# Performance work log

Measured on AMD Instinct MI355X. Metric: run time of the kernel, lower is better.

The kernel has to match this reference:

```python
import jax, jax.numpy as jnp
import numpy as np

C = 1024      # channels
K = 7         # kernel_size
G = 1         # groups (G>1 crashes in the original torch code; see notes)
GC = C // G   # group_channels
OFFSET_SCALE = 2.0
LN_EPS = 1e-5


def setup_inputs() -> dict:
    key = jax.random.key(0)
    ks = jax.random.split(key, 8)
    N, L = 4, 2048
    s = 1.0 / np.sqrt(C)
    x = jax.random.normal(ks[0], (N, L, C), jnp.float32)
    Wi = jax.random.normal(ks[1], (C, C), jnp.float32) * s
    bi = jnp.zeros((C,), jnp.float32)
    dw_w = jax.random.normal(ks[2], (C, 1, 3), jnp.float32) * 0.5   # depthwise conv kernel (O, I/g=1, W)
    dw_b = jnp.zeros((C,), jnp.float32)
    ln_g = jnp.ones((C,), jnp.float32)
    ln_b = jnp.zeros((C,), jnp.float32)
    Wo = jax.random.normal(ks[3], (G * K, C), jnp.float32) * 0.02   # offset head (nonzero to exercise gather)
    bo = jnp.zeros((G * K,), jnp.float32)
    Wm = jax.random.normal(ks[4], (G * K, C), jnp.float32) * 0.02   # mask head
    bm = jnp.zeros((G * K,), jnp.float32)
    Wout = jax.random.normal(ks[5], (C, C), jnp.float32) * s
    bout = jnp.zeros((C,), jnp.float32)
    return {"x": x, "Wi": Wi, "bi": bi, "dw_w": dw_w, "dw_b": dw_b,
            "ln_g": ln_g, "ln_b": ln_b, "Wo": Wo, "bo": bo,
            "Wm": Wm, "bm": bm, "Wout": Wout, "bout": bout}


def _forward(x, Wi, bi, dw_w, dw_b, ln_g, ln_b, Wo, bo, Wm, bm, Wout, bout):
    N, L, Cc = x.shape
    dt = x.dtype
    # input projection
    x_proj = x @ Wi.T + bi                                  # [N,L,C]
    # depthwise conv (k=3, pad=1, groups=C) -> LayerNorm(C) -> GELU(exact)
    y = jax.lax.conv_general_dilated(
        x.transpose(0, 2, 1), dw_w, window_strides=(1,), padding=((1, 1),),
        dimension_numbers=("NCH", "OIH", "NCH"), feature_group_count=Cc)
    x_dw = y.transpose(0, 2, 1) + dw_b                       # [N,L,C]
    mu = x_dw.mean(-1, keepdims=True)
    var = ((x_dw - mu) ** 2).mean(-1, keepdims=True)
    x_dw = (x_dw - mu) * jax.lax.rsqrt(var + LN_EPS) * ln_g + ln_b
    x_dw = jax.nn.gelu(x_dw, approximate=False)
    # dynamic offsets and sampling mask
    offsets = (x_dw @ Wo.T + bo).reshape(N, L, G, K) * OFFSET_SCALE
    mask = jax.nn.softmax((x_dw @ Wm.T + bm).reshape(N, L, G, K), axis=-1)
    mask = jnp.nan_to_num(mask, nan=0.0)
    # absolute sampling positions
    ref_off = jnp.linspace(-(K // 2), K // 2, K).astype(dt)          # [K]
    pos = jnp.arange(L, dtype=dt)[None, :, None, None]               # [1,L,1,1]
    abs_pos = pos + ref_off[None, None, None, :] + offsets           # [N,L,G,K]
    apc = jnp.clip(abs_pos, 0.0, L - 1)
    p_floor = jnp.clip(apc.astype(jnp.int32), 0, L - 1)
    p_ceil = jnp.clip(p_floor + 1, 0, L - 1)
    w_ceil = apc - p_floor.astype(dt)
    w_floor = 1.0 - w_ceil
    valid = jnp.logical_not((abs_pos < 0) | (abs_pos > L - 1)).astype(dt)
    w_floor = w_floor * valid
    w_ceil = w_ceil * valid
    # gather + bilinear blend (G=1: each sample index grabs the full C channels)
    idx_f = p_floor.reshape(N, -1)[:, :, None]                       # [N, L*G*K, 1]
    idx_c = p_ceil.reshape(N, -1)[:, :, None]
    v_floor = jnp.take_along_axis(x_proj, idx_f, axis=1).reshape(N, L, G, K, GC)
    v_ceil = jnp.take_along_axis(x_proj, idx_c, axis=1).reshape(N, L, G, K, GC)
    sampled = v_floor * w_floor[..., None] + v_ceil * w_ceil[..., None]
    out = (sampled * mask[..., None]).sum(axis=3).reshape(N, L, Cc)  # sum over K
    return out @ Wout.T + bout


def reference(x, Wi, bi, dw_w, dw_b, ln_g, ln_b, Wo, bo, Wm, bm, Wout, bout):
    return _forward(x, Wi, bi, dw_w, dw_b, ln_g, ln_b, Wo, bo, Wm, bm, Wout, bout)
```

## Files before the change

### kernel.cpp

```cpp
#include <hip/hip_runtime.h>
#include <hip/hip_bf16.h>
#include <cstdint>

#define C_DIM 1024
#define L_DIM 2048
#define N_DIM 4
#define M_DIM (N_DIM * L_DIM)

typedef __attribute__((ext_vector_type(8))) short frag8;
typedef __attribute__((ext_vector_type(4)))  float f32x4;
typedef __attribute__((ext_vector_type(16))) float f32x16;

__device__ __forceinline__ void gl_lds16(const void* g, void* l) {
  __builtin_amdgcn_global_load_lds((const __attribute__((address_space(1))) void*)g,
                                   (__attribute__((address_space(3))) void*)l,
                                   16, 0, 0);
}
__device__ __forceinline__ void store_out(float* Y, size_t idx, float v) { Y[idx] = v; }
__device__ __forceinline__ void store_out(__hip_bfloat16* Y, size_t idx, float v) {
  Y[idx] = __float2bfloat16(v);
}
__device__ __forceinline__ float4 ldbf4(const __hip_bfloat16* p) {
  union { short4 s; __hip_bfloat16 h[4]; } u; u.s = *(const short4*)p;
  return make_float4((float)u.h[0], (float)u.h[1], (float)u.h[2], (float)u.h[3]);
}
__device__ __forceinline__ void stbf4(__hip_bfloat16* p, float4 v) {
  union { short4 s; __hip_bfloat16 h[4]; } u;
  u.h[0] = __float2bfloat16(v.x); u.h[1] = __float2bfloat16(v.y);
  u.h[2] = __float2bfloat16(v.z); u.h[3] = __float2bfloat16(v.w);
  *(short4*)p = u.s;
}
__device__ __forceinline__ float gelu_fast(float t) {
  const float t3 = t * t * t;
  const float ns = -1.5957691216f * t - 0.0713548163f * t3;
  return t / (1.f + __expf(ns));
}

__global__ __launch_bounds__(256)
void cvt_f32_bf16(const float* __restrict__ in, __hip_bfloat16* __restrict__ out, int n8) {
  const int i = blockIdx.x * 256 + threadIdx.x;
  if (i >= n8) return;
  const float4 a = *(const float4*)(in + (size_t)i * 8);
  const float4 b = *(const float4*)(in + (size_t)i * 8 + 4);
  union { __hip_bfloat16 h[8]; int4 q; } u;
  u.h[0] = __float2bfloat16(a.x); u.h[1] = __float2bfloat16(a.y);
  u.h[2] = __float2bfloat16(a.z); u.h[3] = __float2bfloat16(a.w);
  u.h[4] = __float2bfloat16(b.x); u.h[5] = __float2bfloat16(b.y);
  u.h[6] = __float2bfloat16(b.z); u.h[7] = __float2bfloat16(b.w);
  *(int4*)(out + (size_t)i * 8) = u.q;
}

__global__ __launch_bounds__(256)
void cvt_two_f32_bf16(const float* __restrict__ inA, __hip_bfloat16* __restrict__ outA,
                      const float* __restrict__ inB, __hip_bfloat16* __restrict__ outB,
                      int n8each) {
  int i = blockIdx.x * 256 + threadIdx.x;
  const float* in; __hip_bfloat16* out;
  if (i < n8each) { in = inA; out = outA; }
  else            { in = inB; out = outB; i -= n8each; }
  if (i >= n8each) return;
  const float4 a = *(const float4*)(in + (size_t)i * 8);
  const float4 b = *(const float4*)(in + (size_t)i * 8 + 4);
  union { __hip_bfloat16 h[8]; int4 q; } u;
  u.h[0] = __float2bfloat16(a.x); u.h[1] = __float2bfloat16(a.y);
  u.h[2] = __float2bfloat16(a.z); u.h[3] = __float2bfloat16(a.w);
  u.h[4] = __float2bfloat16(b.x); u.h[5] = __float2bfloat16(b.y);
  u.h[6] = __float2bfloat16(b.z); u.h[7] = __float2bfloat16(b.w);
  *(int4*)(out + (size_t)i * 8) = u.q;
}

template <typename TY>
__global__ __launch_bounds__(256, 2)
void gemm_db(const __hip_bfloat16* __restrict__ X,
             const __hip_bfloat16* __restrict__ W,
             const float* __restrict__ bias,
             TY* __restrict__ Y, int M, int N, int K,
             const float* __restrict__ sArr, const float* __restrict__ bvec)
{
  __shared__ __hip_bfloat16 As[2][2][128 * 32];
  __shared__ __hip_bfloat16 Bs[2][2][128 * 32];
  const int tid  = threadIdx.x;
  const int lane = tid & 63;
  const int wave = tid >> 6;
  const int bm = blockIdx.x * 128;
  const int bn = blockIdx.y * 128;
  const int wr = (wave >> 1) * 64;
  const int wc = (wave & 1) * 64;
  const int srow  = tid >> 2;
  const int skoff = (tid & 3) * 8;

  const __hip_bfloat16* gA0 = X + (size_t)(bm + srow) * K + skoff;
  const __hip_bfloat16* gA1 = X + (size_t)(bm + 64 + srow) * K + skoff;
  const __hip_bfloat16* gB0 = W + (size_t)(bn + srow) * K + skoff;
  const __hip_bfloat16* gB1 = W + (size_t)(bn + 64 + srow) * K + skoff;

  f32x16 acc[2][2] = {};
  const int arow  = lane & 31;
  const int akoff = (lane >> 5) * 8;

#define STAGE(k0, buf)                                        \
  do {                                                        \
    gl_lds16(gA0 + (k0),      &As[buf][0][tid * 8]);          \
    gl_lds16(gA1 + (k0),      &As[buf][0][2048 + tid * 8]);   \
    gl_lds16(gA0 + (k0) + 32, &As[buf][1][tid * 8]);          \
    gl_lds16(gA1 + (k0) + 32, &As[buf][1][2048 + tid * 8]);   \
    gl_lds16(gB0 + (k0),      &Bs[buf][0][tid * 8]);          \
    gl_lds16(gB1 + (k0),      &Bs[buf][0][2048 + tid * 8]);   \
    gl_lds16(gB0 + (k0) + 32, &Bs[buf][1][tid * 8]);          \
    gl_lds16(gB1 + (k0) + 32, &Bs[buf][1][2048 + tid * 8]);   \
  } while (0)

  STAGE(0, 0);
  __syncthreads();
  const int iters = K / 64;
  for (int it = 0; it < iters; ++it) {
    const int cur = it & 1;
    if (it + 1 < iters) STAGE((it + 1) * 64, cur ^ 1);

#pragma unroll
    for (int p = 0; p < 2; ++p)
#pragma unroll
      for (int h = 0; h < 2; ++h) {
        const frag8 a0 = *(const frag8*)&As[cur][p][(wr + arow) * 32 + h * 16 + akoff];
        const frag8 a1 = *(const frag8*)&As[cur][p][(wr + 32 + arow) * 32 + h * 16 + akoff];
        const frag8 b0 = *(const frag8*)&Bs[cur][p][(wc + arow) * 32 + h * 16 + akoff];
        const frag8 b1 = *(const frag8*)&Bs[cur][p][(wc + 32 + arow) * 32 + h * 16 + akoff];
        acc[0][0] = __builtin_amdgcn_mfma_f32_32x32x16_bf16(a0, b0, acc[0][0], 0, 0, 0);
        acc[0][1] = __builtin_amdgcn_mfma_f32_32x32x16_bf16(a0, b1, acc[0][1], 0, 0, 0);
        acc[1][0] = __builtin_amdgcn_mfma_f32_32x32x16_bf16(a1, b0, acc[1][0], 0, 0, 0);
        acc[1][1] = __builtin_amdgcn_mfma_f32_32x32x16_bf16(a1, b1, acc[1][1], 0, 0, 0);
      }
    __syncthreads();
  }
#undef STAGE

#pragma unroll
  for (int i = 0; i < 2; i++)
#pragma unroll
    for (int j = 0; j < 2; j++) {
      const int col = bn + wc + j * 32 + (lane & 31);
      const float bv  = bias ? bias[col] : 0.f;
      const float bvv = (sArr && bvec) ? bvec[col] : 0.f;
#pragma unroll
      for (int r = 0; r < 16; r++) {
        const int row = bm + wr + i * 32 + (r & 3) + 8 * (r >> 2) + 4 * (lane >> 5);
        float extra = bv;
        if (sArr) extra += sArr[row] * bvv;
        store_out(Y, (size_t)row * N + col, acc[i][j][r] + extra);
      }
    }
}

struct Ld8f { float4 a, b; };
struct Ld8b { int4 a; };
__device__ __forceinline__ Ld8f ld8(const float* p) {
  return { *(const float4*)p, *(const float4*)(p + 4) };
}
__device__ __forceinline__ Ld8b ld8(const __hip_bfloat16* p) { return { *(const int4*)p }; }
__device__ __forceinline__ void st8(__hip_bfloat16* l, const Ld8f& v) {
  union { __hip_bfloat16 h[8]; int4 q; } u;
  u.h[0] = __float2bfloat16(v.a.x); u.h[1] = __float2bfloat16(v.a.y);
  u.h[2] = __float2bfloat16(v.a.z); u.h[3] = __float2bfloat16(v.a.w);
  u.h[4] = __float2bfloat16(v.b.x); u.h[5] = __float2bfloat16(v.b.y);
  u.h[6] = __float2bfloat16(v.b.z); u.h[7] = __float2bfloat16(v.b.w);
  *(int4*)l = u.q;
}
__device__ __forceinline__ void st8(__hip_bfloat16* l, const Ld8b& v) { *(int4*)l = v.a; }

template <typename TX, typename TY>
__global__ __launch_bounds__(256, 2)
void gemm_nt(const TX* __restrict__ X, const float* __restrict__ W,
             const float* __restrict__ bias, TY* __restrict__ Y, int M, int N, int K)
{
  __shared__ __hip_bfloat16 As[128 * 32];
  __shared__ __hip_bfloat16 Bs[128 * 32];
  const int tid  = threadIdx.x;
  const int lane = tid & 63;
  const int wave = tid >> 6;
  const int bm = blockIdx.x * 128;
  const int bn = blockIdx.y * 128;
  const int wr = (wave >> 1) * 64;
  const int wc = (wave & 1) * 64;
  const int srow  = tid >> 2;
  const int skoff = (tid & 3) * 8;

  f32x4 acc[4][4] = {};
  const TX*    gA0 = X + (size_t)(bm + srow) * K + skoff;
  const TX*    gA1 = X + (size_t)(bm + 64 + srow) * K + skoff;
  const float* gB0 = W + (size_t)(bn + srow) * K + skoff;
  const float* gB1 = W + (size_t)(bn + 64 + srow) * K + skoff;
  const int arow  = lane & 15;
  const int akoff = (lane >> 4) * 8;

  for (int k0 = 0; k0 < K; k0 += 32) {
    const auto va0 = ld8(gA0 + k0);
    const auto va1 = ld8(gA1 + k0);
    const auto vb0 = ld8(gB0 + k0);
    const auto vb1 = ld8(gB1 + k0);
    __syncthreads();
    st8(&As[srow * 32 + skoff],        va0);
    st8(&As[(64 + srow) * 32 + skoff], va1);
    st8(&Bs[srow * 32 + skoff],        vb0);
    st8(&Bs[(64 + srow) * 32 + skoff], vb1);
    __syncthreads();

    frag8 a[4], b[4];
#pragma unroll
    for (int i = 0; i < 4; i++)
      a[i] = *(const frag8*)&As[(wr + i * 16 + arow) * 32 + akoff];
#pragma unroll
    for (int j = 0; j < 4; j++)
      b[j] = *(const frag8*)&Bs[(wc + j * 16 + arow) * 32 + akoff];
#pragma unroll
    for (int i = 0; i < 4; i++)
#pragma unroll
      for (int j = 0; j < 4; j++)
        acc[i][j] = __builtin_amdgcn_mfma_f32_16x16x32_bf16(a[i], b[j], acc[i][j], 0, 0, 0);
  }
#pragma unroll
  for (int i = 0; i < 4; i++)
#pragma unroll
    for (int j = 0; j < 4; j++) {
      const int col = bn + wc + j * 16 + (lane & 15);
      const float bv = bias[col];
#pragma unroll
      for (int r = 0; r < 4; r++) {
        const int row = bm + wr + i * 16 + (lane >> 4) * 4 + r;
        store_out(Y, (size_t)row * N + col, acc[i][j][r] + bv);
      }
    }
}

__global__ __launch_bounds__(256, 2)
void pre_aux(const float* __restrict__ x,
             const float* __restrict__ dw_w, const float* __restrict__ dw_b,
             const float* __restrict__ ln_g, const float* __restrict__ ln_b,
             const float* __restrict__ Wo,   const float* __restrict__ bo,
             const float* __restrict__ Wm,   const float* __restrict__ bmb,
             const float* __restrict__ Wi,   const float* __restrict__ Wout,
             const float* __restrict__ bi,
             __hip_bfloat16* __restrict__ xbb,
             float* __restrict__ coef,
             __hip_bfloat16* __restrict__ WiT,
             __hip_bfloat16* __restrict__ Woutb,
             float* __restrict__ bvec)
{
  __shared__ float smem[16384];
  const int blk  = blockIdx.x;
  const int tid  = threadIdx.x;
  const int lane = tid & 63;
  const int wid  = tid >> 6;

  if (blk < 256) {
    float (*tile)[65] = (float(*)[65])smem;
    const int bi_ = blk >> 4;
    const int bj  = blk & 15;
    const int r   = tid >> 2;
    const int c0  = (tid & 3) * 16;
    const float* src = Wi + (size_t)(bi_ * 64 + r) * C_DIM + bj * 64 + c0;
    *(float4*)&tile[r][c0]      = *(const float4*)(src);
    *(float4*)&tile[r][c0 + 4]  = *(const float4*)(src + 4);
    *(float4*)&tile[r][c0 + 8]  = *(const float4*)(src + 8);
    *(float4*)&tile[r][c0 + 12] = *(const float4*)(src + 12);
    __syncthreads();
    __hip_bfloat16* dst = WiT + (size_t)(bj * 64 + r) * C_DIM + bi_ * 64 + c0;
    union { __hip_bfloat16 h[16]; int4 q[2]; } u;
#pragma unroll
    for (int i = 0; i < 16; i++) u.h[i] = __float2bfloat16(tile[c0 + i][r]);
    *(int4*)(dst)     = u.q[0];
    *(int4*)(dst + 8) = u.q[1];
    return;
  }
  if (blk < 512) {
    const size_t base = ((size_t)(blk - 256) * 256 + tid) * 16;
#pragma unroll
    for (int h = 0; h < 2; h++) {
      const float4 a = *(const float4*)(Wout + base + h * 8);
      const float4 c = *(const float4*)(Wout + base + h * 8 + 4);
      union { __hip_bfloat16 h8[8]; int4 q; } u;
      u.h8[0] = __float2bfloat16(a.x); u.h8[1] = __float2bfloat16(a.y);
      u.h8[2] = __float2bfloat16(a.z); u.h8[3] = __float2bfloat16(a.w);
      u.h8[4] = __float2bfloat16(c.x); u.h8[5] = __float2bfloat16(c.y);
      u.h8[6] = __float2bfloat16(c.z); u.h8[7] = __float2bfloat16(c.w);
      *(int4*)(Woutb + base + h * 8) = u.q;
    }
    return;
  }
  if (blk < 768) {
    const int row = (blk - 512) * 4 + wid;
    const float* wr_ = Wout + (size_t)row * C_DIM;
    float s = 0.f;
#pragma unroll
    for (int c = 0; c < 4; c++) {
      const int j = c * 256 + lane * 4;
      const float4 w  = *(const float4*)(wr_ + j);
      const float4 bb = *(const float4*)(bi + j);
      s += w.x * bb.x + w.y * bb.y + w.z * bb.z + w.w * bb.w;
    }
#pragma unroll
    for (int m = 1; m < 64; m <<= 1) s += __shfl_xor(s, m);
    if (lane == 0) bvec[row] = s;
    return;
  }

  float* sWo  = smem;
  float* sWm  = smem + 7168;
  float* slng = smem + 14336;
  float* slnb = smem + 15360;

#pragma unroll
  for (int i = 0; i < 7; i++)
    gl_lds16(Wo + (size_t)(i * 256 + tid) * 4, &sWo[(i * 256 + tid) * 4]);
#pragma unroll
  for (int i = 0; i < 7; i++)
    gl_lds16(Wm + (size_t)(i * 256 + tid) * 4, &sWm[(i * 256 + tid) * 4]);
  gl_lds16(ln_g + (size_t)tid * 4, &slng[tid * 4]);
  gl_lds16(ln_b + (size_t)tid * 4, &slnb[tid * 4]);
  __syncthreads();

  const int b    = blk - 768;
  const int bs   = (b & 7) * 64 + (b >> 3);
  const int row0 = bs * 16 + wid * 4;
  const int l0   = row0 & (L_DIM - 1);

  const float* xr = x + (size_t)row0 * C_DIM;

  float4 v[4][4];
#pragma unroll
  for (int j = 0; j < 4; j++) {
    const int c4 = j * 256 + lane * 4;
    float4 xv[6];
#pragma unroll
    for (int m = 0; m < 6; m++) {
      const int lm = l0 + m - 1;
      if (lm >= 0 && lm < L_DIM)
        xv[m] = *(const float4*)(xr + ((long)m - 1) * C_DIM + c4);
      else
        xv[m] = make_float4(0.f, 0.f, 0.f, 0.f);
    }
#pragma unroll
    for (int r = 0; r < 4; r++)
      stbf4(xbb + (size_t)(row0 + r) * C_DIM + c4, xv[r + 1]);

    const float4 w0 = *(const float4*)(dw_w + (size_t)c4 * 3);
    const float4 w1 = *(const float4*)(dw_w + (size_t)c4 * 3 + 4);
    const float4 w2 = *(const float4*)(dw_w + (size_t)c4 * 3 + 8);
    const float4 bb = *(const float4*)(dw_b + c4);
#pragma unroll
    for (int r = 0; r < 4; r++) {
      const float4 xm = xv[r], x0 = xv[r + 1], xq = xv[r + 2];
      v[r][j].x = xm.x * w0.x + x0.x * w0.y + xq.x * w0.z + bb.x;
      v[r][j].y = xm.y * w0.w + x0.y * w1.x + xq.y * w1.y + bb.y;
      v[r][j].z = xm.z * w1.z + x0.z * w1.w + xq.z * w2.x + bb.z;
      v[r][j].w = xm.w * w2.y + x0.w * w2.z + xq.w * w2.w + bb.w;
    }
  }

  float mu[4], rstd[4];
#pragma unroll
  for (int r = 0; r < 4; r++) {
    float s1 = 0.f, s2 = 0.f;
#pragma unroll
    for (int j = 0; j < 4; j++) {
      s1 += v[r][j].x + v[r][j].y + v[r][j].z + v[r][j].w;
      s2 += v[r][j].x * v[r][j].x + v[r][j].y * v[r][j].y
          + v[r][j].z * v[r][j].z + v[r][j].w * v[r][j].w;
    }
    const float t1 = s1 + __shfl_xor(s1, 32);
    const float t2 = s2 + __shfl_xor(s2, 32);
    float cc = (lane < 32) ? t1 : t2;
#pragma unroll
    for (int m = 16; m >= 1; m >>= 1) cc += __shfl_xor(cc, m);
    const float dd = __shfl_xor(cc, 32);
    const float S1 = (lane < 32) ? cc : dd;
    const float S2 = (lane < 32) ? dd : cc;
    mu[r]   = S1 * (1.f / C_DIM);
    rstd[r] = rsqrtf(S2 * (1.f / C_DIM) - mu[r] * mu[r] + 1e-5f);
  }

  float po[4][7] = {}, pm[4][7] = {};
#pragma unroll
  for (int j = 0; j < 4; j++) {
    const int c4 = j * 256 + lane * 4;
    const float4 gg = *(const float4*)&slng[c4];
    const float4 bb = *(const float4*)&slnb[c4];
    float4 g[4];
#pragma unroll
    for (int r = 0; r < 4; r++) {
      g[r].x = gelu_fast((v[r][j].x - mu[r]) * rstd[r] * gg.x + bb.x);
      g[r].y = gelu_fast((v[r][j].y - mu[r]) * rstd[r] * gg.y + bb.y);
      g[r].z = gelu_fast((v[r][j].z - mu[r]) * rstd[r] * gg.z + bb.z);
      g[r].w = gelu_fast((v[r][j].w - mu[r]) * rstd[r] * gg.w + bb.w);
    }
#pragma unroll
    for (int k = 0; k < 7; k++) {
      const float4 wo = *(const float4*)&sWo[k * 1024 + c4];
      const float4 wm = *(const float4*)&sWm[k * 1024 + c4];
#pragma unroll
      for (int r = 0; r < 4; r++) {
        po[r][k] += g[r].x * wo.x + g[r].y * wo.y + g[r].z * wo.z + g[r].w * wo.w;
        pm[r][k] += g[r].x * wm.x + g[r].y * wm.y + g[r].z * wm.z + g[r].w * wm.w;
      }
    }
  }

  float poS[4][7], pmS[4][7];
#pragma unroll
  for (int r = 0; r < 4; r++)
#pragma unroll
    for (int k = 0; k < 7; k++) {
      const float tp = po[r][k] + __shfl_xor(po[r][k], 32);
      const float tm = pm[r][k] + __shfl_xor(pm[r][k], 32);
      float cc = (lane < 32) ? tp : tm;
#pragma unroll
      for (int m = 16; m >= 1; m >>= 1) cc += __shfl_xor(cc, m);
      const float dd = __shfl_xor(cc, 32);
      poS[r][k] = (lane < 32) ? cc : dd;
      pmS[r][k] = (lane < 32) ? dd : cc;
    }

#pragma unroll
  for (int r = 0; r < 4; r++) {
    float lg[7], mx = -1e30f;
#pragma unroll
    for (int k = 0; k < 7; k++) { lg[k] = pmS[r][k] + bmb[k]; mx = fmaxf(mx, lg[k]); }
    float se = 0.f, e[7];
#pragma unroll
    for (int k = 0; k < 7; k++) { e[k] = __expf(lg[k] - mx); se += e[k]; }
    const float inv = 1.f / se;
    const int l = l0 + r;

    if (lane == r) {
      float pk[32];
#pragma unroll
      for (int k = 0; k < 7; k++) {
        const float msk = e[k] * inv;
        const float off = (poS[r][k] + bo[k]) * 2.0f;
        const float ap  = (float)l + (float)(k - 3) + off;
        const float apc = fminf(fmaxf(ap, 0.f), (float)(L_DIM - 1));
        int f = (int)apc;
        int c = f + 1; if (c > L_DIM - 1) c = L_DIM - 1;
        const float w1  = apc - (float)f;
        const float val = (ap < 0.f || ap > (float)(L_DIM - 1)) ? 0.f : 1.f;
        pk[k]      = (1.f - w1) * val * msk;
        pk[8 + k]  = w1 * val * msk;
        pk[16 + k] = (float)f;
        pk[24 + k] = (float)c;
      }
      pk[7] = pk[15] = pk[23] = pk[31] = 0.f;
      float* cr = coef + (size_t)(row0 + r) * 32;
#pragma unroll
      for (int q = 0; q < 8; q++)
        *(float4*)(cr + q * 4) = make_float4(pk[q*4], pk[q*4+1], pk[q*4+2], pk[q*4+3]);
    }
  }
}

__global__ __launch_bounds__(256, 2)
void wcomb_gather2(const __hip_bfloat16* __restrict__ Woutb,
                   const __hip_bfloat16* __restrict__ WiT,
                   __hip_bfloat16* __restrict__ Wcb,
                   const float* __restrict__ coef,
                   const __hip_bfloat16* __restrict__ xbb,
                   __hip_bfloat16* __restrict__ gb,
                   float* __restrict__ sArr)
{
  __shared__ __hip_bfloat16 sm[2][2][128 * 32];
  const int tid  = threadIdx.x;
  const int lane = tid & 63;
  const int wid  = tid >> 6;

  if (blockIdx.x < 64) {
    const int bm = (int)(blockIdx.x >> 3) * 128;
    const int bn = (int)(blockIdx.x & 7) * 128;
    const int wr = (wid >> 1) * 64;
    const int wc = (wid & 1) * 64;
    const int K  = C_DIM;
    const int r0  = tid >> 2;
    const int kc0 = (tid & 3) * 8;
    const __hip_bfloat16* gA = Woutb + (size_t)bm * K;
    const __hip_bfloat16* gB = WiT   + (size_t)bn * K;

#define W2STAGE(k0, buf)                                                          \
    do {                                                                          \
      gl_lds16(gA + (size_t)r0 * K + (k0) + kc0,        &sm[buf][0][tid * 8]);    \
      gl_lds16(gA + (size_t)(r0 + 64) * K + (k0) + kc0, &sm[buf][0][2048 + tid * 8]); \
      gl_lds16(gB + (size_t)r0 * K + (k0) + kc0,        &sm[buf][1][tid * 8]);    \
      gl_lds16(gB + (size_t)(r0 + 64) * K + (k0) + kc0, &sm[buf][1][2048 + tid * 8]); \
    } while (0)

    f32x16 acc[2][2] = {};
    const int arow  = lane & 31;
    const int akoff = (lane >> 5) * 8;

    W2STAGE(0, 0);
    __syncthreads();
    for (int it = 0; it < 32; ++it) {
      const int cur = it & 1;
      if (it + 1 < 32) W2STAGE((it + 1) * 32, cur ^ 1);
#pragma unroll
      for (int h = 0; h < 2; ++h) {
        const frag8 a0 = *(const frag8*)&sm[cur][0][(wr + arow) * 32 + h * 16 + akoff];
        const frag8 a1 = *(const frag8*)&sm[cur][0][(wr + 32 + arow) * 32 + h * 16 + akoff];
        const frag8 b0 = *(const frag8*)&sm[cur][1][(wc + arow) * 32 + h * 16 + akoff];
        const frag8 b1 = *(const frag8*)&sm[cur][1][(wc + 32 + arow) * 32 + h * 16 + akoff];
        acc[0][0] = __builtin_amdgcn_mfma_f32_32x32x16_bf16(a0, b0, acc[0][0], 0, 0, 0);
        acc[0][1] = __builtin_amdgcn_mfma_f32_32x32x16_bf16(a0, b1, acc[0][1], 0, 0, 0);
        acc[1][0] = __builtin_amdgcn_mfma_f32_32x32x16_bf16(a1, b0, acc[1][0], 0, 0, 0);
        acc[1][1] = __builtin_amdgcn_mfma_f32_32x32x16_bf16(a1, b1, acc[1][1], 0, 0, 0);
      }
      __syncthreads();
    }
#undef W2STAGE

#pragma unroll
    for (int i = 0; i < 2; i++)
#pragma unroll
      for (int j = 0; j < 2; j++) {
        const int col = bn + wc + j * 32 + (lane & 31);
#pragma unroll
        for (int r = 0; r < 16; r++) {
          const int row = bm + wr + i * 32 + (r & 3) + 8 * (r >> 2) + 4 * (lane >> 5);
          Wcb[(size_t)row * C_DIM + col] = __float2bfloat16(acc[i][j][r]);
        }
      }
    return;
  }

  const int b   = (int)blockIdx.x - 64;
  const int bs  = (b & 7) * 256 + (b >> 3);
  const int row = bs * 4 + wid;
  const int n   = row >> 11;

  const float* cr = coef + (size_t)row * 32;
  const float4 q0 = *(const float4*)(cr);
  const float4 q1 = *(const float4*)(cr + 4);
  const float4 q2 = *(const float4*)(cr + 8);
  const float4 q3 = *(const float4*)(cr + 12);
  const float4 q4 = *(const float4*)(cr + 16);
  const float4 q5 = *(const float4*)(cr + 20);
  const float4 q6 = *(const float4*)(cr + 24);
  const float4 q7 = *(const float4*)(cr + 28);

  const float wf[7] = {q0.x, q0.y, q0.z, q0.w, q1.x, q1.y, q1.z};
  const float wc[7] = {q2.x, q2.y, q2.z, q2.w, q3.x, q3.y, q3.z};
  const int   pf[7] = {(int)q4.x, (int)q4.y, (int)q4.z, (int)q4.w, (int)q5.x, (int)q5.y, (int)q5.z};
  const int   pc[7] = {(int)q6.x, (int)q6.y, (int)q6.z, (int)q6.w, (int)q7.x, (int)q7.y, (int)q7.z};

  if (lane == 0) {
    sArr[row] = q0.x + q0.y + q0.z + q0.w + q1.x + q1.y + q1.z
              + q2.x + q2.y + q2.z + q2.w + q3.x + q3.y + q3.z;
  }

  const __hip_bfloat16* xpn = xbb + ((size_t)n * L_DIM) * C_DIM;
  __hip_bfloat16* so = gb + (size_t)row * C_DIM;

#pragma unroll
  for (int j = 0; j < 2; j++) {
    const int c8 = j * 512 + lane * 8;
    float a[8] = {0.f, 0.f, 0.f, 0.f, 0.f, 0.f, 0.f, 0.f};
#pragma unroll
    for (int k = 0; k < 7; k++) {
      union { int4 q; __hip_bfloat16 h[8]; } uf, uc;
      uf.q = *(const int4*)(xpn + (size_t)pf[k] * C_DIM + c8);
      uc.q = *(const int4*)(xpn + (size_t)pc[k] * C_DIM + c8);
#pragma unroll
      for (int t = 0; t < 8; t++)
        a[t] += wf[k] * (float)uf.h[t] + wc[k] * (float)uc.h[t];
    }
    union { int4 q; __hip_bfloat16 h[8]; } uo;
#pragma unroll
    for (int t = 0; t < 8; t++) uo.h[t] = __float2bfloat16(a[t]);
    *(int4*)(so + c8) = uo.q;
  }
}

__global__ __launch_bounds__(256)
void mid_fused_v4(const float* __restrict__ x,
                  const float* __restrict__ dw_w, const float* __restrict__ dw_b,
                  const float* __restrict__ ln_g, const float* __restrict__ ln_b,
                  const float* __restrict__ Wo,   const float* __restrict__ bo,
                  const float* __restrict__ Wm,   const float* __restrict__ bmb,
                  const __hip_bfloat16* __restrict__ xp,
                  __hip_bfloat16* __restrict__ smp)
{
  const int b    = blockIdx.x;
  const int bs   = (b & 7) * 256 + (b >> 3);
  const int wid  = threadIdx.x >> 6;
  const int lane = threadIdx.x & 63;
  const int row  = bs * 4 + wid;
  const int l    = row & (L_DIM - 1);
  const int n    = row >> 11;

  const float* xr = x + (size_t)row * C_DIM;

  float4 v[4];
#pragma unroll
  for (int j = 0; j < 4; j++) {
    const int c4 = j * 256 + lane * 4;
    const float4 x0 = *(const float4*)(xr + c4);
    float4 xm = make_float4(0.f, 0.f, 0.f, 0.f);
    float4 xq = make_float4(0.f, 0.f, 0.f, 0.f);
    if (l > 0)         xm = *(const float4*)(xr + c4 - C_DIM);
    if (l < L_DIM - 1) xq = *(const float4*)(xr + c4 + C_DIM);
    const float4 w0 = *(const float4*)(dw_w + (size_t)c4 * 3);
    const float4 w1 = *(const float4*)(dw_w + (size_t)c4 * 3 + 4);
    const float4 w2 = *(const float4*)(dw_w + (size_t)c4 * 3 + 8);
    const float4 bb = *(const float4*)(dw_b + c4);
    v[j].x = xm.x * w0.x + x0.x * w0.y + xq.x * w0.z + bb.x;
    v[j].y = xm.y * w0.w + x0.y * w1.x + xq.y * w1.y + bb.y;
    v[j].z = xm.z * w1.z + x0.z * w1.w + xq.z * w2.x + bb.z;
    v[j].w = xm.w * w2.y + x0.w * w2.z + xq.w * w2.w + bb.w;
  }

  float s1 = 0.f, s2 = 0.f;
#pragma unroll
  for (int j = 0; j < 4; j++) {
    s1 += v[j].x + v[j].y + v[j].z + v[j].w;
    s2 += v[j].x * v[j].x + v[j].y * v[j].y + v[j].z * v[j].z + v[j].w * v[j].w;
  }
#pragma unroll
  for (int m = 1; m < 64; m <<= 1) { s1 += __shfl_xor(s1, m); s2 += __shfl_xor(s2, m); }
  const float mu   = s1 * (1.f / C_DIM);
  const float rstd = rsqrtf(s2 * (1.f / C_DIM) - mu * mu + 1e-5f);

  float4 g[4];
#pragma unroll
  for (int j = 0; j < 4; j++) {
    const int c4 = j * 256 + lane * 4;
    const float4 gg = *(const float4*)(ln_g + c4);
    const float4 bb = *(const float4*)(ln_b + c4);
    g[j].x = gelu_fast((v[j].x - mu) * rstd * gg.x + bb.x);
    g[j].y = gelu_fast((v[j].y - mu) * rstd * gg.y + bb.y);
    g[j].z = gelu_fast((v[j].z - mu) * rstd * gg.z + bb.z);
    g[j].w = gelu_fast((v[j].w - mu) * rstd * gg.w + bb.w);
  }

  float po[7] = {0,0,0,0,0,0,0}, pm[7] = {0,0,0,0,0,0,0};
#pragma unroll
  for (int k = 0; k < 7; k++) {
#pragma unroll
    for (int j = 0; j < 4; j++) {
      const int c4 = j * 256 + lane * 4;
      const float4 wo = *(const float4*)(Wo + (size_t)k * C_DIM + c4);
      const float4 wm = *(const float4*)(Wm + (size_t)k * C_DIM + c4);
      po[k] += g[j].x * wo.x + g[j].y * wo.y + g[j].z * wo.z + g[j].w * wo.w;
      pm[k] += g[j].x * wm.x + g[j].y * wm.y + g[j].z * wm.z + g[j].w * wm.w;
    }
  }
#pragma unroll
  for (int k = 0; k < 7; k++)
#pragma unroll
    for (int m = 1; m < 64; m <<= 1) {
      po[k] += __shfl_xor(po[k], m);
      pm[k] += __shfl_xor(pm[k], m);
    }

  float lg[7], mx = -1e30f;
#pragma unroll
  for (int k = 0; k < 7; k++) { lg[k] = pm[k] + bmb[k]; mx = fmaxf(mx, lg[k]); }
  float se = 0.f, e[7];
#pragma unroll
  for (int k = 0; k < 7; k++) { e[k] = __expf(lg[k] - mx); se += e[k]; }
  const float inv = 1.f / se;

  float wf[7], wcl[7]; int pf[7], pc[7];
#pragma unroll
  for (int k = 0; k < 7; k++) {
    const float msk = e[k] * inv;
    const float off = (po[k] + bo[k]) * 2.0f;
    const float ap  = (float)l + (float)(k - 3) + off;
    const float apc = fminf(fmaxf(ap, 0.f), (float)(L_DIM - 1));
    int f = (int)apc;
    int c = f + 1; if (c > L_DIM - 1) c = L_DIM - 1;
    const float w1  = apc - (float)f;
    const float val = (ap < 0.f || ap > (float)(L_DIM - 1)) ? 0.f : 1.f;
    wf[k]  = (1.f - w1) * val * msk;
    wcl[k] = w1 * val * msk;
    pf[k] = f; pc[k] = c;
  }

  const __hip_bfloat16* xpn = xp + ((size_t)n * L_DIM) * C_DIM;
  __hip_bfloat16* so = smp + (size_t)row * C_DIM;
#pragma unroll
  for (int j = 0; j < 4; j++) {
    const int c4 = j * 256 + lane * 4;
    float4 a = make_float4(0.f, 0.f, 0.f, 0.f);
#pragma unroll
    for (int k = 0; k < 7; k++) {
      const float4 vf = ldbf4(xpn + (size_t)pf[k] * C_DIM + c4);
      const float4 vc = ldbf4(xpn + (size_t)pc[k] * C_DIM + c4);
      a.x += wf[k] * vf.x + wcl[k] * vc.x;
      a.y += wf[k] * vf.y + wcl[k] * vc.y;
      a.z += wf[k] * vf.z + wcl[k] * vc.z;
      a.w += wf[k] * vf.w + wcl[k] * vc.w;
    }
    stbf4(so + c4, a);
  }
}

extern "C" void kernel_launch(void* const* d_in, const int* in_sizes, int n_in,
                              void* d_out, int out_size, void* d_ws, size_t ws_size,
                              hipStream_t stream)
{
  const float* x    = (const float*)d_in[0];
  const float* Wi   = (const float*)d_in[1];
  const float* bi   = (const float*)d_in[2];
  const float* dw_w = (const float*)d_in[3];
  const float* dw_b = (const float*)d_in[4];
  const float* ln_g = (const float*)d_in[5];
  const float* ln_b = (const float*)d_in[6];
  const float* Wo   = (const float*)d_in[7];
  const float* bo   = (const float*)d_in[8];
  const float* Wm   = (const float*)d_in[9];
  const float* bm   = (const float*)d_in[10];
  const float* Wout = (const float*)d_in[11];
  const float* bout = (const float*)d_in[12];
  float* out = (float*)d_out;

  const size_t XE = (size_t)M_DIM * C_DIM;
  const size_t WE = (size_t)C_DIM * C_DIM;
  char* wsb = (char*)d_ws;

  __hip_bfloat16* xbb2  = (__hip_bfloat16*)wsb;
  __hip_bfloat16* gb    = (__hip_bfloat16*)(wsb + XE * 2);
  __hip_bfloat16* Woutb2= (__hip_bfloat16*)(wsb + XE * 4);
  __hip_bfloat16* WiT   = (__hip_bfloat16*)(wsb + XE * 4 + WE * 2);
  __hip_bfloat16* Wcb   = (__hip_bfloat16*)(wsb + XE * 4 + WE * 4);
  float* coef2 = (float*)(wsb + XE * 4 + WE * 6);
  float* sArr  = (float*)(wsb + XE * 4 + WE * 6 + (size_t)M_DIM * 128);
  float* bvec  = (float*)(wsb + XE * 4 + WE * 6 + (size_t)M_DIM * 128 + (size_t)M_DIM * 4);
  const size_t need_v5 = XE * 4 + WE * 6 + (size_t)M_DIM * 132 + 4096;

  __hip_bfloat16* xp    = (__hip_bfloat16*)wsb;
  __hip_bfloat16* smp   = (__hip_bfloat16*)(wsb + XE * 2);
  __hip_bfloat16* Wib   = (__hip_bfloat16*)(wsb + XE * 4);
  __hip_bfloat16* Woutb = (__hip_bfloat16*)(wsb + XE * 4 + WE * 2);
  __hip_bfloat16* xbb   = (__hip_bfloat16*)(wsb + XE * 4 + WE * 4);
  const size_t need_w2   = XE * 4 + WE * 4;
  const size_t need_full = need_w2 + XE * 2;

  dim3 gg(M_DIM / 128, C_DIM / 128);

  if (ws_size >= need_v5) {
    pre_aux<<<1280, 256, 0, stream>>>(
        x, dw_w, dw_b, ln_g, ln_b, Wo, bo, Wm, bm,
        Wi, Wout, bi, xbb2, coef2, WiT, Woutb2, bvec);
    wcomb_gather2<<<2112, 256, 0, stream>>>(
        Woutb2, WiT, Wcb, coef2, xbb2, gb, sArr);
    gemm_db<float><<<gg, 256, 0, stream>>>(
        gb, Wcb, bout, out, M_DIM, C_DIM, C_DIM, sArr, bvec);
  } else if (ws_size >= need_full) {
    cvt_f32_bf16<<<(int)(XE / 8 / 256), 256, 0, stream>>>(x, xbb, (int)(XE / 8));
    cvt_two_f32_bf16<<<(int)(2 * (WE / 8) / 256), 256, 0, stream>>>(
        Wi, Wib, Wout, Woutb, (int)(WE / 8));
    gemm_db<__hip_bfloat16><<<gg, 256, 0, stream>>>(xbb, Wib, bi, xp, M_DIM, C_DIM, C_DIM,
                                                    nullptr, nullptr);
    mid_fused_v4<<<M_DIM / 4, 256, 0, stream>>>(x, dw_w, dw_b, ln_g, ln_b, Wo, bo, Wm, bm, xp, smp);
    gemm_db<float><<<gg, 256, 0, stream>>>(smp, Woutb, bout, out, M_DIM, C_DIM, C_DIM,
                                           nullptr, nullptr);
  } else if (ws_size >= need_w2) {
    cvt_f32_bf16<<<(int)(WE / 8 / 256), 256, 0, stream>>>(Wout, Woutb, (int)(WE / 8));
    gemm_nt<float, __hip_bfloat16><<<gg, 256, 0, stream>>>(x, Wi, bi, xp, M_DIM, C_DIM, C_DIM);
    mid_fused_v4<<<M_DIM / 4, 256, 0, stream>>>(x, dw_w, dw_b, ln_g, ln_b, Wo, bo, Wm, bm, xp, smp);
    gemm_db<float><<<gg, 256, 0, stream>>>(smp, Woutb, bout, out, M_DIM, C_DIM, C_DIM,
                                           nullptr, nullptr);
  } else {
    gemm_nt<float, __hip_bfloat16><<<gg, 256, 0, stream>>>(x, Wi, bi, xp, M_DIM, C_DIM, C_DIM);
    mid_fused_v4<<<M_DIM / 4, 256, 0, stream>>>(x, dw_w, dw_b, ln_g, ln_b, Wo, bo, Wm, bm, xp, smp);
    gemm_nt<__hip_bfloat16, float><<<gg, 256, 0, stream>>>(smp, Wout, bout, out, M_DIM, C_DIM, C_DIM);
  }
}
```

Before: 180.6 us.

## Shrink pre_aux LDS and per-wave rows to raise occupancy

The aux section of pre_aux now handles 2 rows per wave instead of 4, doubling its block count. It also stages the offset and mask head weights through one shared LDS buffer in sequence instead of holding both at once, cutting LDS from 64KB to 36KB and raising launch bounds to 4 blocks per CU. The aim is higher occupancy and lower register pressure to hide memory latency, at the cost of two extra barriers and a second weight load per block. Each block also reloads weights for fewer rows, and each row's 3-tap convolution now fetches 2 rows of x instead of 1.5.

```diff
diff --git a/kernel.cpp b/kernel.cpp
--- a/kernel.cpp
+++ b/kernel.cpp
@@ -231,7 +231,7 @@
     }
 }
 
-__global__ __launch_bounds__(256, 2)
+__global__ __launch_bounds__(256, 4)
 void pre_aux(const float* __restrict__ x,
              const float* __restrict__ dw_w, const float* __restrict__ dw_b,
              const float* __restrict__ ln_g, const float* __restrict__ ln_b,
@@ -245,7 +245,7 @@
              __hip_bfloat16* __restrict__ Woutb,
              float* __restrict__ bvec)
 {
-  __shared__ float smem[16384];
+  __shared__ float smem[9216];
   const int blk  = blockIdx.x;
   const int tid  = threadIdx.x;
   const int lane = tid & 63;
@@ -303,35 +303,30 @@
     return;
   }
 
-  float* sWo  = smem;
-  float* sWm  = smem + 7168;
-  float* slng = smem + 14336;
-  float* slnb = smem + 15360;
+  float* sW   = smem;
+  float* slng = smem + 7168;
+  float* slnb = smem + 8192;
 
 #pragma unroll
   for (int i = 0; i < 7; i++)
-    gl_lds16(Wo + (size_t)(i * 256 + tid) * 4, &sWo[(i * 256 + tid) * 4]);
-#pragma unroll
-  for (int i = 0; i < 7; i++)
-    gl_lds16(Wm + (size_t)(i * 256 + tid) * 4, &sWm[(i * 256 + tid) * 4]);
+    gl_lds16(Wo + (size_t)(i * 256 + tid) * 4, &sW[(i * 256 + tid) * 4]);
   gl_lds16(ln_g + (size_t)tid * 4, &slng[tid * 4]);
   gl_lds16(ln_b + (size_t)tid * 4, &slnb[tid * 4]);
-  __syncthreads();
 
   const int b    = blk - 768;
-  const int bs   = (b & 7) * 64 + (b >> 3);
-  const int row0 = bs * 16 + wid * 4;
+  const int bs   = (b & 7) * 128 + (b >> 3);
+  const int row0 = bs * 8 + wid * 2;
   const int l0   = row0 & (L_DIM - 1);
 
   const float* xr = x + (size_t)row0 * C_DIM;
 
-  float4 v[4][4];
+  float4 v[2][4];
 #pragma unroll
   for (int j = 0; j < 4; j++) {
     const int c4 = j * 256 + lane * 4;
-    float4 xv[6];
-#pragma unroll
-    for (int m = 0; m < 6; m++) {
+    float4 xv[4];
+#pragma unroll
+    for (int m = 0; m < 4; m++) {
       const int lm = l0 + m - 1;
       if (lm >= 0 && lm < L_DIM)
         xv[m] = *(const float4*)(xr + ((long)m - 1) * C_DIM + c4);
@@ -339,7 +334,7 @@
         xv[m] = make_float4(0.f, 0.f, 0.f, 0.f);
     }
 #pragma unroll
-    for (int r = 0; r < 4; r++)
+    for (int r = 0; r < 2; r++)
       stbf4(xbb + (size_t)(row0 + r) * C_DIM + c4, xv[r + 1]);
 
     const float4 w0 = *(const float4*)(dw_w + (size_t)c4 * 3);
@@ -347,7 +342,7 @@
     const float4 w2 = *(const float4*)(dw_w + (size_t)c4 * 3 + 8);
     const float4 bb = *(const float4*)(dw_b + c4);
 #pragma unroll
-    for (int r = 0; r < 4; r++) {
+    for (int r = 0; r < 2; r++) {
       const float4 xm = xv[r], x0 = xv[r + 1], xq = xv[r + 2];
       v[r][j].x = xm.x * w0.x + x0.x * w0.y + xq.x * w0.z + bb.x;
       v[r][j].y = xm.y * w0.w + x0.y * w1.x + xq.y * w1.y + bb.y;
@@ -356,9 +351,9 @@
     }
   }
 
-  float mu[4], rstd[4];
-#pragma unroll
-  for (int r = 0; r < 4; r++) {
+  float mu[2], rstd[2];
+#pragma unroll
+  for (int r = 0; r < 2; r++) {
     float s1 = 0.f, s2 = 0.f;
 #pragma unroll
     for (int j = 0; j < 4; j++) {
@@ -378,35 +373,58 @@
     rstd[r] = rsqrtf(S2 * (1.f / C_DIM) - mu[r] * mu[r] + 1e-5f);
   }
 
-  float po[4][7] = {}, pm[4][7] = {};
+  __syncthreads();
+
 #pragma unroll
   for (int j = 0; j < 4; j++) {
     const int c4 = j * 256 + lane * 4;
     const float4 gg = *(const float4*)&slng[c4];
     const float4 bb = *(const float4*)&slnb[c4];
-    float4 g[4];
-#pragma unroll
-    for (int r = 0; r < 4; r++) {
-      g[r].x = gelu_fast((v[r][j].x - mu[r]) * rstd[r] * gg.x + bb.x);
-      g[r].y = gelu_fast((v[r][j].y - mu[r]) * rstd[r] * gg.y + bb.y);
-      g[r].z = gelu_fast((v[r][j].z - mu[r]) * rstd[r] * gg.z + bb.z);
-      g[r].w = gelu_fast((v[r][j].w - mu[r]) * rstd[r] * gg.w + bb.w);
-    }
+#pragma unroll
+    for (int r = 0; r < 2; r++) {
+      v[r][j].x = gelu_fast((v[r][j].x - mu[r]) * rstd[r] * gg.x + bb.x);
+      v[r][j].y = gelu_fast((v[r][j].y - mu[r]) * rstd[r] * gg.y + bb.y);
+      v[r][j].z = gelu_fast((v[r][j].z - mu[r]) * rstd[r] * gg.z + bb.z);
+      v[r][j].w = gelu_fast((v[r][j].w - mu[r]) * rstd[r] * gg.w + bb.w);
+    }
+  }
+
+  float po[2][7] = {};
+#pragma unroll
+  for (int j = 0; j < 4; j++) {
+    const int c4 = j * 256 + lane * 4;
 #pragma unroll
     for (int k = 0; k < 7; k++) {
-      const float4 wo = *(const float4*)&sWo[k * 1024 + c4];
-      const float4 wm = *(const float4*)&sWm[k * 1024 + c4];
-#pragma unroll
-      for (int r = 0; r < 4; r++) {
-        po[r][k] += g[r].x * wo.x + g[r].y * wo.y + g[r].z * wo.z + g[r].w * wo.w;
-        pm[r][k] += g[r].x * wm.x + g[r].y * wm.y + g[r].z * wm.z + g[r].w * wm.w;
-      }
-    }
-  }
-
-  float poS[4][7], pmS[4][7];
-#pragma unroll
-  for (int r = 0; r < 4; r++)
+      const float4 wo = *(const float4*)&sW[k * 1024 + c4];
+#pragma unroll
+      for (int r = 0; r < 2; r++)
+        po[r][k] += v[r][j].x * wo.x + v[r][j].y * wo.y
+                  + v[r][j].z * wo.z + v[r][j].w * wo.w;
+    }
+  }
+
+  __syncthreads();
+#pragma unroll
+  for (int i = 0; i < 7; i++)
+    gl_lds16(Wm + (size_t)(i * 256 + tid) * 4, &sW[(i * 256 + tid) * 4]);
+  __syncthreads();
+
+  float pm[2][7] = {};
+#pragma unroll
+  for (int j = 0; j < 4; j++) {
+    const int c4 = j * 256 + lane * 4;
+#pragma unroll
+    for (int k = 0; k < 7; k++) {
+      const float4 wm = *(const float4*)&sW[k * 1024 + c4];
+#pragma unroll
+      for (int r = 0; r < 2; r++)
+        pm[r][k] += v[r][j].x * wm.x + v[r][j].y * wm.y
+                  + v[r][j].z * wm.z + v[r][j].w * wm.w;
+    }
+  }
+
+#pragma unroll
+  for (int r = 0; r < 2; r++)
 #pragma unroll
     for (int k = 0; k < 7; k++) {
       const float tp = po[r][k] + __shfl_xor(po[r][k], 32);
@@ -415,15 +433,15 @@
 #pragma unroll
       for (int m = 16; m >= 1; m >>= 1) cc += __shfl_xor(cc, m);
       const float dd = __shfl_xor(cc, 32);
-      poS[r][k] = (lane < 32) ? cc : dd;
-      pmS[r][k] = (lane < 32) ? dd : cc;
-    }
-
-#pragma unroll
-  for (int r = 0; r < 4; r++) {
+      po[r][k] = (lane < 32) ? cc : dd;
+      pm[r][k] = (lane < 32) ? dd : cc;
+    }
+
+#pragma unroll
+  for (int r = 0; r < 2; r++) {
     float lg[7], mx = -1e30f;
 #pragma unroll
-    for (int k = 0; k < 7; k++) { lg[k] = pmS[r][k] + bmb[k]; mx = fmaxf(mx, lg[k]); }
+    for (int k = 0; k < 7; k++) { lg[k] = pm[r][k] + bmb[k]; mx = fmaxf(mx, lg[k]); }
     float se = 0.f, e[7];
 #pragma unroll
     for (int k = 0; k < 7; k++) { e[k] = __expf(lg[k] - mx); se += e[k]; }
@@ -435,7 +453,7 @@
 #pragma unroll
       for (int k = 0; k < 7; k++) {
         const float msk = e[k] * inv;
-        const float off = (poS[r][k] + bo[k]) * 2.0f;
+        const float off = (po[r][k] + bo[k]) * 2.0f;
         const float ap  = (float)l + (float)(k - 3) + off;
         const float apc = fminf(fmaxf(ap, 0.f), (float)(L_DIM - 1));
         int f = (int)apc;
@@ -743,7 +761,7 @@
   dim3 gg(M_DIM / 128, C_DIM / 128);
 
   if (ws_size >= need_v5) {
-    pre_aux<<<1280, 256, 0, stream>>>(
+    pre_aux<<<1792, 256, 0, stream>>>(
         x, dw_w, dw_b, ln_g, ln_b, Wo, bo, Wm, bm,
         Wi, Wout, bi, xbb2, coef2, WiT, Woutb2, bvec);
     wcomb_gather2<<<2112, 256, 0, stream>>>(
```

Result: slower. 218.7 us (+21.1%).
